# Performance work log

Measured on AMD Instinct MI355X. Metric: run time of the kernel, lower is better.

Reference implementation:

```python
import jax, jax.numpy as jnp
import numpy as np

EPS = 1e-5


def _dwconv(x, w, pad):
    # x: [N,C,H,W]; w: [C,1,k,k] depthwise kernel (groups = C)
    return jax.lax.conv_general_dilated(
        x, w, window_strides=(1, 1), padding=[(pad, pad), (pad, pad)],
        feature_group_count=w.shape[0],
        dimension_numbers=("NCHW", "OIHW", "NCHW"))


def _bn(y, g, b, m, v):
    # inference-mode BatchNorm2d using running stats; per-channel affine
    scale = (g / jnp.sqrt(v + EPS))[None, :, None, None]
    shift = (b - m * g / jnp.sqrt(v + EPS))[None, :, None, None]
    return y * scale + shift


def setup_inputs() -> dict:
    key = jax.random.key(0)
    ks = jax.random.split(key, 16)
    C, KL, KS = 384, 13, 3
    N, H, W = 16, 64, 64
    inp = {
        "x": jax.random.normal(ks[0], (N, C, H, W), jnp.float32),
        "w_large": jax.random.normal(ks[1], (C, 1, KL, KL), jnp.float32) * 0.05,
        "w_small": jax.random.normal(ks[2], (C, 1, KS, KS), jnp.float32) * 0.2,
        "g_l": jax.random.normal(ks[3], (C,), jnp.float32),
        "b_l": jax.random.normal(ks[4], (C,), jnp.float32),
        "m_l": jax.random.normal(ks[5], (C,), jnp.float32),
        "v_l": jax.random.uniform(ks[6], (C,), jnp.float32, 0.5, 1.5),
        "g_s": jax.random.normal(ks[7], (C,), jnp.float32),
        "b_s": jax.random.normal(ks[8], (C,), jnp.float32),
        "m_s": jax.random.normal(ks[9], (C,), jnp.float32),
        "v_s": jax.random.uniform(ks[10], (C,), jnp.float32, 0.5, 1.5),
        "g_i": jax.random.normal(ks[11], (C,), jnp.float32),
        "b_i": jax.random.normal(ks[12], (C,), jnp.float32),
        "m_i": jax.random.normal(ks[13], (C,), jnp.float32),
        "v_i": jax.random.uniform(ks[14], (C,), jnp.float32, 0.5, 1.5),
    }
    return inp


def reference(x, w_large, w_small, g_l, b_l, m_l, v_l,
              g_s, b_s, m_s, v_s, g_i, b_i, m_i, v_i):
    kl = w_large.shape[-1]
    ks = w_small.shape[-1]
    out = (_bn(_dwconv(x, w_large, kl // 2), g_l, b_l, m_l, v_l)
           + _bn(_dwconv(x, w_small, ks // 2), g_s, b_s, m_s, v_s)
           + _bn(x, g_i, b_i, m_i, v_i))
    return out
```

## Files before the change

kernel.cpp:

```cpp
#include <hip/hip_runtime.h>

#define EPSV 1e-5f

typedef __fp16 f16x8 __attribute__((ext_vector_type(8)));
typedef float f32x4 __attribute__((ext_vector_type(4)));
typedef __fp16 half2v __attribute__((ext_vector_type(2)));

__device__ __forceinline__ unsigned h2_as_u32(half2v h) {
    union { half2v h; unsigned u; } cv;
    cv.h = h;
    return cv.u;
}

#define LROWS 76
#define LSTRIDE 88

__global__ __launch_bounds__(256) void fuse_weights(
    const float* __restrict__ w_large, const float* __restrict__ w_small,
    const float* __restrict__ g_l, const float* __restrict__ b_l,
    const float* __restrict__ m_l, const float* __restrict__ v_l,
    const float* __restrict__ g_s, const float* __restrict__ b_s,
    const float* __restrict__ m_s, const float* __restrict__ v_s,
    const float* __restrict__ g_i, const float* __restrict__ b_i,
    const float* __restrict__ m_i, const float* __restrict__ v_i,
    float* __restrict__ bf, uint4* __restrict__ wB) {
    __shared__ float sw[169];
    const int c = blockIdx.x;
    const int t = threadIdx.x;
    const float sl = g_l[c] * rsqrtf(v_l[c] + EPSV);
    const float ss = g_s[c] * rsqrtf(v_s[c] + EPSV);
    const float si = g_i[c] * rsqrtf(v_i[c] + EPSV);
    if (t < 169) {
        const int ky = t / 13, kx = t % 13;
        float w = w_large[c * 169 + t] * sl;
        if (ky >= 5 && ky <= 7 && kx >= 5 && kx <= 7)
            w += w_small[c * 9 + (ky - 5) * 3 + (kx - 5)] * ss;
        if (t == 6 * 13 + 6) w += si;
        sw[t] = w;
    }
    if (t == 0)
        bf[c] = (b_l[c] - m_l[c] * sl) + (b_s[c] - m_s[c] * ss) +
                (b_i[c] - m_i[c] * si);
    __syncthreads();
    for (int it = t; it < 832; it += 256) {
        const int dy = it >> 6;
        const int l = it & 63;
        const int i = l & 15;
        const int kb = (l >> 4) * 8;
        unsigned u[4];
#pragma unroll
        for (int jj = 0; jj < 4; ++jj) {
            const int kx0 = kb + 2 * jj - i - 2;
            const int kx1 = kx0 + 1;
            const float w0 =
                (kx0 >= 0 && kx0 <= 12) ? sw[dy * 13 + kx0] : 0.0f;
            const float w1 =
                (kx1 >= 0 && kx1 <= 12) ? sw[dy * 13 + kx1] : 0.0f;
            u[jj] = h2_as_u32(__builtin_amdgcn_cvt_pkrtz(w0, w1));
        }
        wB[(size_t)c * 832 + it] = make_uint4(u[0], u[1], u[2], u[3]);
    }
}

__global__ __launch_bounds__(256, 4) void dwconv_mfma(
    const float* __restrict__ x, const uint4* __restrict__ wB,
    const float* __restrict__ bf, float* __restrict__ out) {
    __shared__ __align__(16) __fp16 tile[LROWS * LSTRIDE];

    const int t = threadIdx.x;
    const int img = blockIdx.x;
    const int c = __builtin_amdgcn_readfirstlane(img % 384);
    const size_t base = (size_t)img * 4096;

    unsigned* tz = (unsigned*)tile;
    for (int i2 = t; i2 < LROWS * LSTRIDE / 2; i2 += 256) tz[i2] = 0u;
    __syncthreads();

    {
        const int r = t >> 2;
        const int q = t & 3;
        const float* src = x + base + r * 64 + q * 16;
        unsigned u[8];
#pragma unroll
        for (int p = 0; p < 4; ++p) {
            const float4 v = ((const float4*)src)[p];
            u[2 * p + 0] = h2_as_u32(__builtin_amdgcn_cvt_pkrtz(v.x, v.y));
            u[2 * p + 1] = h2_as_u32(__builtin_amdgcn_cvt_pkrtz(v.z, v.w));
        }
        unsigned* dst = tz + (r + 6) * 44 + 4 + q * 8;
        *(uint4*)dst = make_uint4(u[0], u[1], u[2], u[3]);
        *(uint4*)(dst + 4) = make_uint4(u[4], u[5], u[6], u[7]);
    }

    const int l = t & 63;
    const int wv = t >> 6;
    f16x8 Bf[13];
    {
        const uint4* wbp = wB + (size_t)c * 832 + l;
#pragma unroll
        for (int dy = 0; dy < 13; ++dy) {
            union { uint4 u; f16x8 h; } cv;
            cv.u = wbp[dy * 64];
            Bf[dy] = cv.h;
        }
    }
    const float bv = bf[c];
    __syncthreads();

    const int c0 = wv * 16;
    const int lrow = l & 15;
    const int kb = (l >> 4) * 8;
    const __fp16* abase = tile + lrow * LSTRIDE + c0 + kb;

    const int ocol = c0 + (l & 15);
    const int orow = 4 * (l >> 4);

#pragma unroll 1
    for (int rp = 0; rp < 2; ++rp) {
        const int r0a = rp * 32;
        const int r0b = rp * 32 + 16;
        f32x4 accA = {bv, bv, bv, bv};
        f32x4 accB = {bv, bv, bv, bv};
#pragma unroll
        for (int dy = 0; dy < 13; ++dy) {
            const f16x8 a0 = *(const f16x8*)(abase + (r0a + dy) * LSTRIDE);
            const f16x8 a1 = *(const f16x8*)(abase + (r0b + dy) * LSTRIDE);
            accA = __builtin_amdgcn_mfma_f32_16x16x32_f16(a0, Bf[dy], accA,
                                                          0, 0, 0);
            accB = __builtin_amdgcn_mfma_f32_16x16x32_f16(a1, Bf[dy], accB,
                                                          0, 0, 0);
        }
        float* ob = out + base;
#pragma unroll
        for (int q = 0; q < 4; ++q) {
            ob[(r0a + orow + q) * 64 + ocol] = accA[q];
            ob[(r0b + orow + q) * 64 + ocol] = accB[q];
        }
    }
}

extern "C" void kernel_launch(void* const* d_in, const int* in_sizes, int n_in,
                              void* d_out, int out_size, void* d_ws,
                              size_t ws_size, hipStream_t stream) {
    const float* x = (const float*)d_in[0];
    const float* w_large = (const float*)d_in[1];
    const float* w_small = (const float*)d_in[2];
    const float* g_l = (const float*)d_in[3];
    const float* b_l = (const float*)d_in[4];
    const float* m_l = (const float*)d_in[5];
    const float* v_l = (const float*)d_in[6];
    const float* g_s = (const float*)d_in[7];
    const float* b_s = (const float*)d_in[8];
    const float* m_s = (const float*)d_in[9];
    const float* v_s = (const float*)d_in[10];
    const float* g_i = (const float*)d_in[11];
    const float* b_i = (const float*)d_in[12];
    const float* m_i = (const float*)d_in[13];
    const float* v_i = (const float*)d_in[14];
    float* outp = (float*)d_out;

    float* bfp = (float*)d_ws;
    uint4* wB = (uint4*)(bfp + 384);

    fuse_weights<<<384, 256, 0, stream>>>(w_large, w_small, g_l, b_l, m_l, v_l,
                                          g_s, b_s, m_s, v_s, g_i, b_i, m_i,
                                          v_i, bfp, wB);
    dwconv_mfma<<<16 * 384, 256, 0, stream>>>(x, wB, bfp, outp);
}
```

Baseline: 41.87 us.

## Give each wave a private haloed LDS strip and drop block barriers

Each wave now loads its own 16-column output strip plus an 8-column halo on each side, converting to fp16 and writing zeros for out-of-bounds positions directly. This removes the separate LDS zero-fill pass and both __syncthreads barriers. The row loop is fully unrolled into four independent MFMA accumulator chains for more instruction-level parallelism. In exchange, each wave rereads overlapping halo columns from global memory, total LDS use grows, and more accumulator registers are live at once.

```diff
diff --git a/kernel.cpp b/kernel.cpp
--- a/kernel.cpp
+++ b/kernel.cpp
@@ -13,7 +13,8 @@
 }
 
 #define LROWS 76
-#define LSTRIDE 88
+#define WSTRU 20
+#define WREGU (LROWS * WSTRU)
 
 __global__ __launch_bounds__(256) void fuse_weights(
     const float* __restrict__ w_large, const float* __restrict__ w_small,
@@ -65,77 +66,80 @@
 __global__ __launch_bounds__(256, 4) void dwconv_mfma(
     const float* __restrict__ x, const uint4* __restrict__ wB,
     const float* __restrict__ bf, float* __restrict__ out) {
-    __shared__ __align__(16) __fp16 tile[LROWS * LSTRIDE];
+    __shared__ __align__(16) unsigned lds[4 * WREGU];
 
     const int t = threadIdx.x;
     const int img = blockIdx.x;
     const int c = __builtin_amdgcn_readfirstlane(img % 384);
     const size_t base = (size_t)img * 4096;
 
-    unsigned* tz = (unsigned*)tile;
-    for (int i2 = t; i2 < LROWS * LSTRIDE / 2; i2 += 256) tz[i2] = 0u;
-    __syncthreads();
+    const int l = t & 63;
+    const int wv = t >> 6;
+    unsigned* __restrict__ wlds = lds + wv * WREGU;
+    const int xc0 = 16 * wv - 8;
 
-    {
-        const int r = t >> 2;
-        const int q = t & 3;
-        const float* src = x + base + r * 64 + q * 16;
-        unsigned u[8];
+    const uint4* __restrict__ wbp = wB + (size_t)c * 832 + l;
+    f16x8 Bf[13];
 #pragma unroll
-        for (int p = 0; p < 4; ++p) {
-            const float4 v = ((const float4*)src)[p];
-            u[2 * p + 0] = h2_as_u32(__builtin_amdgcn_cvt_pkrtz(v.x, v.y));
-            u[2 * p + 1] = h2_as_u32(__builtin_amdgcn_cvt_pkrtz(v.z, v.w));
+    for (int dy = 0; dy < 13; ++dy) {
+        union { uint4 u; f16x8 h; } cv;
+        cv.u = wbp[dy * 64];
+        Bf[dy] = cv.h;
+    }
+    const float bv = bf[c];
+
+#pragma unroll
+    for (int i = 0; i < 5; ++i) {
+        const int idx = 64 * i + l;
+        if (idx < 304) {
+            const int row = idx >> 2;
+            const int q = idx & 3;
+            const int xr = row - 6;
+            const int xc = xc0 + 8 * q;
+            uint4 val = make_uint4(0u, 0u, 0u, 0u);
+            if (((unsigned)xr < 64u) && ((unsigned)xc < 64u)) {
+                const float4* sp = (const float4*)(x + base + xr * 64 + xc);
+                const float4 v0 = sp[0];
+                const float4 v1 = sp[1];
+                val.x = h2_as_u32(__builtin_amdgcn_cvt_pkrtz(v0.x, v0.y));
+                val.y = h2_as_u32(__builtin_amdgcn_cvt_pkrtz(v0.z, v0.w));
+                val.z = h2_as_u32(__builtin_amdgcn_cvt_pkrtz(v1.x, v1.y));
+                val.w = h2_as_u32(__builtin_amdgcn_cvt_pkrtz(v1.z, v1.w));
+            }
+            *(uint4*)(wlds + row * WSTRU + q * 4) = val;
         }
-        unsigned* dst = tz + (r + 6) * 44 + 4 + q * 8;
-        *(uint4*)dst = make_uint4(u[0], u[1], u[2], u[3]);
-        *(uint4*)(dst + 4) = make_uint4(u[4], u[5], u[6], u[7]);
     }
 
-    const int l = t & 63;
-    const int wv = t >> 6;
-    f16x8 Bf[13];
-    {
-        const uint4* wbp = wB + (size_t)c * 832 + l;
+    const int lrow = l & 15;
+    const int g = l >> 4;
+    const __fp16* abase = (const __fp16*)wlds + lrow * 40 + g * 8;
+
+    f32x4 acc0 = {bv, bv, bv, bv};
+    f32x4 acc1 = {bv, bv, bv, bv};
+    f32x4 acc2 = {bv, bv, bv, bv};
+    f32x4 acc3 = {bv, bv, bv, bv};
+
 #pragma unroll
-        for (int dy = 0; dy < 13; ++dy) {
-            union { uint4 u; f16x8 h; } cv;
-            cv.u = wbp[dy * 64];
-            Bf[dy] = cv.h;
-        }
+    for (int dy = 0; dy < 13; ++dy) {
+        const f16x8 a0 = *(const f16x8*)(abase + (dy) * 40);
+        const f16x8 a1 = *(const f16x8*)(abase + (16 + dy) * 40);
+        const f16x8 a2 = *(const f16x8*)(abase + (32 + dy) * 40);
+        const f16x8 a3 = *(const f16x8*)(abase + (48 + dy) * 40);
+        acc0 = __builtin_amdgcn_mfma_f32_16x16x32_f16(a0, Bf[dy], acc0, 0, 0, 0);
+        acc1 = __builtin_amdgcn_mfma_f32_16x16x32_f16(a1, Bf[dy], acc1, 0, 0, 0);
+        acc2 = __builtin_amdgcn_mfma_f32_16x16x32_f16(a2, Bf[dy], acc2, 0, 0, 0);
+        acc3 = __builtin_amdgcn_mfma_f32_16x16x32_f16(a3, Bf[dy], acc3, 0, 0, 0);
     }
-    const float bv = bf[c];
-    __syncthreads();
 
-    const int c0 = wv * 16;
-    const int lrow = l & 15;
-    const int kb = (l >> 4) * 8;
-    const __fp16* abase = tile + lrow * LSTRIDE + c0 + kb;
-
-    const int ocol = c0 + (l & 15);
+    const int ocol = 16 * wv + (l & 15);
     const int orow = 4 * (l >> 4);
-
-#pragma unroll 1
-    for (int rp = 0; rp < 2; ++rp) {
-        const int r0a = rp * 32;
-        const int r0b = rp * 32 + 16;
-        f32x4 accA = {bv, bv, bv, bv};
-        f32x4 accB = {bv, bv, bv, bv};
+    float* ob = out + base;
 #pragma unroll
-        for (int dy = 0; dy < 13; ++dy) {
-            const f16x8 a0 = *(const f16x8*)(abase + (r0a + dy) * LSTRIDE);
-            const f16x8 a1 = *(const f16x8*)(abase + (r0b + dy) * LSTRIDE);
-            accA = __builtin_amdgcn_mfma_f32_16x16x32_f16(a0, Bf[dy], accA,
-                                                          0, 0, 0);
-            accB = __builtin_amdgcn_mfma_f32_16x16x32_f16(a1, Bf[dy], accB,
-                                                          0, 0, 0);
-        }
-        float* ob = out + base;
-#pragma unroll
-        for (int q = 0; q < 4; ++q) {
-            ob[(r0a + orow + q) * 64 + ocol] = accA[q];
-            ob[(r0b + orow + q) * 64 + ocol] = accB[q];
-        }
+    for (int q = 0; q < 4; ++q) {
+        ob[(orow + q) * 64 + ocol] = acc0[q];
+        ob[(16 + orow + q) * 64 + ocol] = acc1[q];
+        ob[(32 + orow + q) * 64 + ocol] = acc2[q];
+        ob[(48 + orow + q) * 64 + ocol] = acc3[q];
     }
 }
 
```

Result: slower. 44.78 us (+6.9%).
